# Performance work log

Hardware: AMD Instinct MI355X
Metric: run time of the kernel (lower is better)

## Reference

```python
import jax, jax.numpy as jnp
import numpy as np

NH, NKV, D = 16, 8, 128
HID = 2048
EPS = 1e-6
ROPE_BASE = 10000.0
T = 2048


def setup_inputs() -> dict:
    key = jax.random.key(0)
    k1, k2, k3 = jax.random.split(key, 3)
    return {
        "positions": jnp.arange(T, dtype=jnp.int32),
        "hidden_states": jax.random.normal(k1, (T, HID), dtype=jnp.float32),
        "w_qkv": jax.random.normal(k2, (HID, (NH + 2 * NKV) * D), dtype=jnp.float32) * 0.02,
        "w_o": jax.random.normal(k3, (NH * D, HID), dtype=jnp.float32) * 0.02,
        "q_norm_w": jnp.ones((D,), dtype=jnp.float32),
        "k_norm_w": jnp.ones((D,), dtype=jnp.float32),
    }


def _rmsnorm(x, w):
    # per-head RMSNorm over last dim (head_dim)
    return x * jax.lax.rsqrt(jnp.mean(x * x, axis=-1, keepdims=True) + EPS) * w


def reference(positions, hidden_states, w_qkv, w_o, q_norm_w, k_norm_w):
    t = hidden_states.shape[0]
    scale = D ** -0.5

    # fused QKV projection, then split
    qkv = hidden_states @ w_qkv                       # [T, (NH+2*NKV)*D]
    q, k, v = jnp.split(qkv, [NH * D, (NH + NKV) * D], axis=-1)
    q = q.reshape(t, NH, D)
    k = k.reshape(t, NKV, D)
    v = v.reshape(t, NKV, D)

    # per-head QK RMSNorm (Qwen3)
    q = _rmsnorm(q, q_norm_w)
    k = _rmsnorm(k, k_norm_w)

    # RoPE (neox style: rotate half-split pairs)
    inv_freq = 1.0 / (ROPE_BASE ** (jnp.arange(0, D, 2, dtype=jnp.float32) / D))
    freqs = positions.astype(jnp.float32)[:, None] * inv_freq  # [T, D/2]
    cos = jnp.cos(freqs)[:, None, :]                   # [T, 1, D/2]
    sin = jnp.sin(freqs)[:, None, :]

    def rope(x):
        x1, x2 = jnp.split(x, 2, axis=-1)
        return jnp.concatenate([x1 * cos - x2 * sin, x2 * cos + x1 * sin], axis=-1)

    q = rope(q)
    k = rope(k)

    # GQA: repeat kv heads
    g = NH // NKV
    kr = jnp.repeat(k, g, axis=1)                      # [T, NH, D]
    vr = jnp.repeat(v, g, axis=1)

    # causal attention
    scores = jnp.einsum('thd,shd->hts', q, kr) * scale  # [NH, T, T]
    causal = jnp.tril(jnp.ones((t, t), dtype=bool))
    scores = jnp.where(causal[None], scores, -jnp.inf)
    probs = jax.nn.softmax(scores, axis=-1)
    o = jnp.einsum('hts,shd->thd', probs, vr).reshape(t, NH * D)

    return o @ w_o
```

## Files before the change

### kernel.cpp

```cpp
#include <hip/hip_runtime.h>
#include <math.h>

#define T_TOK 2048
#define HIDDEN 2048
#define NH 16
#define NKV 8
#define DH 128

typedef unsigned short u16;
typedef __attribute__((ext_vector_type(8))) short bf16x8;
typedef __attribute__((ext_vector_type(4))) float f32x4;

__device__ __forceinline__ u16 f2bf(float f) {
  union { float f; unsigned u; } x; x.f = f;
  unsigned r = (x.u + 0x7fffu + ((x.u >> 16) & 1u)) >> 16;
  return (u16)r;
}

__device__ __forceinline__ float bf2f(u16 v) {
  union { unsigned u; float f; } x; x.u = ((unsigned)v) << 16;
  return x.f;
}

__device__ __forceinline__ void gload16(const void* g, void* l) {
  __builtin_amdgcn_global_load_lds((const __attribute__((address_space(1))) void*)g,
                                   (__attribute__((address_space(3))) void*)l,
                                   16, 0, 0);
}

__global__ __launch_bounds__(256) void prepass(const float* __restrict__ hidden,
                                               const float* __restrict__ w_qkv,
                                               const float* __restrict__ w_o,
                                               u16* __restrict__ Xb,
                                               u16* __restrict__ WqkvT,
                                               u16* __restrict__ WoT) {
  __shared__ float tile[64][65];
  const int b = blockIdx.x;
  if (b < 4096) {
    int i = b * 256 + threadIdx.x;
    float4 v = ((const float4*)hidden)[i];
    ushort4 o;
    o.x = f2bf(v.x); o.y = f2bf(v.y); o.z = f2bf(v.z); o.w = f2bf(v.w);
    ((ushort4*)Xb)[i] = o;
    return;
  }
  const float* in; u16* out; int R, Cdim, c0, r0;
  if (b < 6144) {
    int bb = b - 4096;
    in = w_qkv; out = WqkvT; R = 2048; Cdim = 4096;
    c0 = (bb & 63) * 64; r0 = (bb >> 6) * 64;
  } else {
    int bb = b - 6144;
    in = w_o; out = WoT; R = 2048; Cdim = 2048;
    c0 = (bb & 31) * 64; r0 = (bb >> 5) * 64;
  }
  const int tx = threadIdx.x & 63, ty = threadIdx.x >> 6;
#pragma unroll
  for (int i = 0; i < 64; i += 4)
    tile[ty + i][tx] = in[(size_t)(r0 + ty + i) * Cdim + c0 + tx];
  __syncthreads();
#pragma unroll
  for (int i = 0; i < 64; i += 4)
    out[(size_t)(c0 + ty + i) * R + r0 + tx] = f2bf(tile[tx][ty + i]);
}

__global__ __launch_bounds__(256) void add_parts2(const u16* __restrict__ a,
                                                  const u16* __restrict__ b,
                                                  float* __restrict__ o, int n4) {
  int i = blockIdx.x * blockDim.x + threadIdx.x;
  if (i < n4) {
    ushort4 x = ((const ushort4*)a)[i], y = ((const ushort4*)b)[i];
    float4 z;
    z.x = bf2f(x.x) + bf2f(y.x);
    z.y = bf2f(x.y) + bf2f(y.y);
    z.z = bf2f(x.z) + bf2f(y.z);
    z.w = bf2f(x.w) + bf2f(y.w);
    ((float4*)o)[i] = z;
  }
}

__global__ __launch_bounds__(256) void rope_vt(const u16* __restrict__ qkv,
                                               const int* __restrict__ pos,
                                               const float* __restrict__ qw,
                                               const float* __restrict__ kw,
                                               u16* __restrict__ Qg,
                                               u16* __restrict__ Kg,
                                               u16* __restrict__ Vt,
                                               unsigned* __restrict__ counter) {
  __shared__ float tile[64][65];
  const int b = blockIdx.x;
  if (b < 12288) {
    const int wave = threadIdx.x >> 6, j = threadIdx.x & 63;
    const int idx = b * 4 + wave;
    const int t = idx & 2047, slot = idx >> 11;
    const float QSC = 0.088388347648318447f * 1.4426950408889634f;
    const size_t base_i = (size_t)t * 4096 + slot * 128;
    float x1 = bf2f(qkv[base_i + j]);
    float x2 = bf2f(qkv[base_i + j + 64]);
    float ss = x1 * x1 + x2 * x2;
#pragma unroll
    for (int m = 1; m < 64; m <<= 1) ss += __shfl_xor(ss, m);
    float r = rsqrtf(ss * (1.0f / 128.0f) + 1e-6f);
    const bool isq = slot < NH;
    const float* w = isq ? qw : kw;
    float xn1 = x1 * r * w[j], xn2 = x2 * r * w[j + 64];
    float fp = (float)pos[t];
    float inv_freq = exp2f(-(float)j * (13.287712379549449f / 64.0f));
    float ang = fp * inv_freq;
    float sn, cs;
    sincosf(ang, &sn, &cs);
    float o1 = xn1 * cs - xn2 * sn;
    float o2 = xn2 * cs + xn1 * sn;
    if (isq) {
      size_t base = ((size_t)slot * T_TOK + t) * DH;
      Qg[base + j] = f2bf(o1 * QSC); Qg[base + 64 + j] = f2bf(o2 * QSC);
    } else {
      size_t base = ((size_t)(slot - NH) * T_TOK + t) * DH;
      Kg[base + j] = f2bf(o1); Kg[base + 64 + j] = f2bf(o2);
    }
    return;
  }
  if (b == 12288 && threadIdx.x == 0) *counter = 0u;
  const int bb = b - 12288;
  const int h = bb & 7, rest = bb >> 3;
  const int t0 = (rest & 31) * 64, d0 = (rest >> 5) * 64;
  const int tx = threadIdx.x & 63, ty = threadIdx.x >> 6;
#pragma unroll
  for (int i = 0; i < 64; i += 4) {
    size_t gi = (size_t)(t0 + ty + i) * 4096 + (NH + NKV) * DH + h * DH + d0 + tx;
    tile[ty + i][tx] = bf2f(qkv[gi]);
  }
  __syncthreads();
#pragma unroll
  for (int i = 0; i < 64; i += 4)
    Vt[((size_t)h * DH + d0 + ty + i) * T_TOK + t0 + tx] = f2bf(tile[tx][ty + i]);
}

__global__ __launch_bounds__(512, 2) void gemm128x256(const u16* __restrict__ A,
                                                      const u16* __restrict__ Bt,
                                                      void* __restrict__ Cout,
                                                      int M, int N, int K,
                                                      int lda, int ldb, int obf16) {
  __shared__ __attribute__((aligned(128))) char lds[98304];

  const int nx = N >> 8, ny = M >> 7;
  const int flat = blockIdx.x;
  const int per = gridDim.x >> 3;
  const int swz = (flat & 7) * per + (flat >> 3);
  const int by = swz % ny;
  const int rest = swz / ny;
  const int bx = rest % nx;
  const int bz = rest / nx;
  const int m0 = by << 7, n0 = bx << 8;
  A += (size_t)bz * K;
  Bt += (size_t)bz * K;

  const int tid = threadIdx.x;
  const int wave = tid >> 6, lane = tid & 63;
  const int l15 = lane & 15, quad = lane >> 4;
  const int wr = wave >> 2, wc = wave & 3;

  size_t aoff;
  {
    int chunk = tid;
    int line = chunk >> 3;
    int ls8 = (chunk & 7) ^ (line & 7);
    int row = line * 2 + (ls8 >> 2);
    int ks = ls8 & 3;
    aoff = (size_t)(m0 + row) * lda + ks * 8;
  }
  size_t boff[2];
#pragma unroll
  for (int c = 0; c < 2; ++c) {
    int chunk = c * 512 + tid;
    int line = chunk >> 3;
    int ls8 = (chunk & 7) ^ (line & 7);
    int row = line * 2 + (ls8 >> 2);
    int ks = ls8 & 3;
    boff[c] = (size_t)(n0 + row) * ldb + ks * 8;
  }

#define STAGE(tt) do {                                                   \
    char* da = lds + ((tt) & 3) * 8192 + wave * 1024;                    \
    char* db = lds + 32768 + ((tt) & 3) * 16384 + wave * 1024;           \
    const int kk = (tt) * 32;                                            \
    gload16(A + aoff + kk, da);                                          \
    gload16(Bt + boff[0] + kk, db);                                      \
    gload16(Bt + boff[1] + kk, db + 8192);                               \
  } while (0)

  const int fragoff = (l15 >> 1) * 128 +
                      (((((l15 & 1) << 2) | quad) ^ ((l15 >> 1) & 7)) << 4);

  const f32x4 zero = {0.f, 0.f, 0.f, 0.f};
  f32x4 acc[4][4];
#pragma unroll
  for (int i = 0; i < 4; ++i)
#pragma unroll
    for (int j = 0; j < 4; ++j) acc[i][j] = zero;

  const int NT = K >> 5;
  STAGE(0); STAGE(1); STAGE(2);
  asm volatile("s_waitcnt vmcnt(6)" ::: "memory");
  __builtin_amdgcn_s_barrier();

  for (int t = 0; t < NT; ++t) {
    const char* As = lds + (t & 3) * 8192 + wr * 4096 + fragoff;
    const char* Bs = lds + 32768 + (t & 3) * 16384 + wc * 4096 + fragoff;
    bf16x8 af[4], bfr[4];
#pragma unroll
    for (int mt = 0; mt < 4; ++mt) af[mt] = *(const bf16x8*)(As + mt * 1024);
#pragma unroll
    for (int nt = 0; nt < 4; ++nt) bfr[nt] = *(const bf16x8*)(Bs + nt * 1024);

    if (t + 3 < NT) STAGE(t + 3);

    __builtin_amdgcn_s_setprio(1);
#pragma unroll
    for (int mt = 0; mt < 4; ++mt)
#pragma unroll
      for (int nt = 0; nt < 4; ++nt)
        acc[mt][nt] = __builtin_amdgcn_mfma_f32_16x16x32_bf16(af[mt], bfr[nt], acc[mt][nt], 0, 0, 0);
    __builtin_amdgcn_s_setprio(0);

    const int rem = NT - 1 - t;
    if (rem >= 3)      asm volatile("s_waitcnt vmcnt(6)" ::: "memory");
    else if (rem == 2) asm volatile("s_waitcnt vmcnt(3)" ::: "memory");
    else if (rem == 1) asm volatile("s_waitcnt vmcnt(0)" ::: "memory");
    if (rem > 0) __builtin_amdgcn_s_barrier();
  }
#undef STAGE

  if (obf16) {
    u16* C = (u16*)Cout + (size_t)bz * M * N;
#pragma unroll
    for (int mt = 0; mt < 4; ++mt)
#pragma unroll
      for (int nt = 0; nt < 4; ++nt)
#pragma unroll
        for (int r = 0; r < 4; ++r)
          C[(size_t)(m0 + wr * 64 + mt * 16 + quad * 4 + r) * N + n0 + wc * 64 + nt * 16 + l15] =
              f2bf(acc[mt][nt][r]);
  } else {
    float* C = (float*)Cout + (size_t)bz * M * N;
#pragma unroll
    for (int mt = 0; mt < 4; ++mt)
#pragma unroll
      for (int nt = 0; nt < 4; ++nt)
#pragma unroll
        for (int r = 0; r < 4; ++r)
          C[(size_t)(m0 + wr * 64 + mt * 16 + quad * 4 + r) * N + n0 + wc * 64 + nt * 16 + l15] =
              acc[mt][nt][r];
  }
}

__global__ __launch_bounds__(256) void attn_kernel(const u16* __restrict__ Qg,
                                                   const u16* __restrict__ Kg,
                                                   const u16* __restrict__ Vtg,
                                                   float* __restrict__ Opart,
                                                   float* __restrict__ Lpart,
                                                   unsigned* __restrict__ counter) {
  __shared__ u16 Klds[2][64 * 128];
  __shared__ u16 Vlds[2][128 * 64];
  __shared__ u16 Plds[4][16 * 72];
  __shared__ unsigned item_s;
  const int wave = threadIdx.x >> 6, lane = threadIdx.x & 63;
  const int l15 = lane & 15, quad = lane >> 4;
  u16* Pw = &Plds[wave][0];
  const f32x4 zero = {0.f, 0.f, 0.f, 0.f};
  const float4 zero4 = {0.f, 0.f, 0.f, 0.f};

#define STAGEKV(jj, sl) do {                                            \
    u16* Kd = &Klds[sl][0]; u16* Vd = &Vlds[sl][0];                     \
    _Pragma("unroll")                                                   \
    for (int c = 0; c < 4; ++c) {                                       \
      int chunk = wave * 4 + c;                                         \
      int sL = chunk * 64 + lane;                                       \
      { int ss = sL >> 4;                                               \
        int g = (sL & 15) ^ (ss & 15);                                  \
        gload16(Kh + ((size_t)((jj) * 64 + ss)) * DH + g * 8, Kd + chunk * 512); } \
      { int d = sL >> 3;                                                \
        int g = (sL & 7) ^ (d & 7);                                     \
        gload16(Vh + (size_t)d * T_TOK + (jj) * 64 + g * 8, Vd + chunk * 512); } \
    } } while (0)

  for (;;) {
    __syncthreads();
    if (threadIdx.x == 0) item_s = atomicAdd(counter, 1u);
    __syncthreads();
    const unsigned item = item_s;
    if (item >= 1024u) break;
    const int qt = 31 - (int)(item >> 5);
    const int s  = (int)(item >> 4) & 1;
    const int h  = (int)item & 15;
    const int kvh = h >> 1;
    const int slot = (h * 32 + qt) * 2 + s;
    const int j0 = s ? (qt + 2) >> 1 : 0;
    const int j1 = s ? qt + 1 : (qt + 2) >> 1;

    float* Oslot = Opart + (size_t)slot * (64 * 128);

    if (j0 >= j1) {
      for (int t = threadIdx.x; t < 64 * 128 / 4; t += 256) ((float4*)Oslot)[t] = zero4;
      if (threadIdx.x < 64) Lpart[slot * 64 + threadIdx.x] = 0.f;
      continue;
    }

    const u16* Qh = Qg + (size_t)h * T_TOK * DH;
    const u16* Kh = Kg + (size_t)kvh * T_TOK * DH;
    const u16* Vh = Vtg + (size_t)kvh * DH * T_TOK;
    const int qrow0 = qt * 64 + wave * 16;

    bf16x8 qf[4];
#pragma unroll
    for (int ks = 0; ks < 4; ++ks)
      qf[ks] = *(const bf16x8*)(Qh + (size_t)(qrow0 + l15) * DH + ks * 32 + quad * 8);

    f32x4 oacc[8];
#pragma unroll
    for (int i = 0; i < 8; ++i) oacc[i] = zero;
    float l_i[4] = {0.f, 0.f, 0.f, 0.f};

    STAGEKV(j0, 0);
    asm volatile("s_waitcnt vmcnt(0)" ::: "memory");
    __builtin_amdgcn_s_barrier();

    for (int j = j0; j < j1; ++j) {
      const int sl = (j - j0) & 1;
      if (j + 1 < j1) STAGEKV(j + 1, sl ^ 1);
      const u16* Kl = &Klds[sl][0];
      const u16* Vl = &Vlds[sl][0];

      f32x4 sacc[4];
#pragma unroll
      for (int nt = 0; nt < 4; ++nt) sacc[nt] = zero;
      __builtin_amdgcn_s_setprio(1);
#pragma unroll
      for (int nt = 0; nt < 4; ++nt) {
        int sr = nt * 16 + l15;
#pragma unroll
        for (int ks = 0; ks < 4; ++ks) {
          bf16x8 kf = *(const bf16x8*)&Kl[sr * 128 + (((ks * 4 + quad) ^ (sr & 15)) * 8)];
          sacc[nt] = __builtin_amdgcn_mfma_f32_16x16x32_bf16(qf[ks], kf, sacc[nt], 0, 0, 0);
        }
      }
      __builtin_amdgcn_s_setprio(0);

      if (j == qt) {
#pragma unroll
        for (int nt = 0; nt < 4; ++nt)
#pragma unroll
          for (int r = 0; r < 4; ++r) {
            int col = j * 64 + nt * 16 + l15;
            int row = qrow0 + quad * 4 + r;
            if (col > row) sacc[nt][r] = -INFINITY;
          }
      }

#pragma unroll
      for (int nt = 0; nt < 4; ++nt)
#pragma unroll
        for (int r = 0; r < 4; ++r) {
          float pv = exp2f(sacc[nt][r]);
          unsigned u = __float_as_uint(pv);
          Pw[(quad * 4 + r) * 72 + nt * 16 + l15] = (u16)(u >> 16);
          l_i[r] += __uint_as_float(u & 0xffff0000u);
        }

      bf16x8 pf[2];
#pragma unroll
      for (int ks = 0; ks < 2; ++ks)
        pf[ks] = *(const bf16x8*)&Pw[l15 * 72 + ks * 32 + quad * 8];
      __builtin_amdgcn_s_setprio(1);
#pragma unroll
      for (int ot = 0; ot < 8; ++ot) {
        int d = ot * 16 + l15;
#pragma unroll
        for (int ks = 0; ks < 2; ++ks) {
          bf16x8 vf = *(const bf16x8*)&Vl[d * 64 + (((ks * 4 + quad) ^ (d & 7)) * 8)];
          oacc[ot] = __builtin_amdgcn_mfma_f32_16x16x32_bf16(pf[ks], vf, oacc[ot], 0, 0, 0);
        }
      }
      __builtin_amdgcn_s_setprio(0);

      if (j + 1 < j1) {
        asm volatile("s_waitcnt vmcnt(0)" ::: "memory");
        __builtin_amdgcn_s_barrier();
      }
    }

#pragma unroll
    for (int ot = 0; ot < 8; ++ot)
#pragma unroll
      for (int r = 0; r < 4; ++r)
        Oslot[(wave * 16 + quad * 4 + r) * 128 + ot * 16 + l15] = oacc[ot][r];
#pragma unroll
    for (int msk = 1; msk < 16; msk <<= 1)
#pragma unroll
      for (int r = 0; r < 4; ++r) l_i[r] += __shfl_xor(l_i[r], msk);
    if (l15 == 0) {
#pragma unroll
      for (int r = 0; r < 4; ++r)
        Lpart[slot * 64 + wave * 16 + quad * 4 + r] = l_i[r];
    }
  }
#undef STAGEKV
}

__global__ __launch_bounds__(256) void attn_merge(const float* __restrict__ Opart,
                                                  const float* __restrict__ Lpart,
                                                  u16* __restrict__ Og) {
  const int b = blockIdx.x;
  const int h = b & 15, qt = b >> 4;
  const int slot0 = (h * 32 + qt) * 2, slot1 = slot0 + 1;
  const float4* O0 = (const float4*)(Opart + (size_t)slot0 * (64 * 128));
  const float4* O1 = (const float4*)(Opart + (size_t)slot1 * (64 * 128));
#pragma unroll
  for (int it = 0; it < 8; ++it) {
    int idx = it * 256 + threadIdx.x;
    int r = idx >> 5, c4 = idx & 31;
    float rl = 1.0f / (Lpart[slot0 * 64 + r] + Lpart[slot1 * 64 + r]);
    float4 a = O0[idx], c = O1[idx];
    int row = qt * 64 + r, col = c4 * 4;
    u16* dst = Og + (size_t)row * (NH * DH) + h * DH + col;
    dst[0] = f2bf((a.x + c.x) * rl);
    dst[1] = f2bf((a.y + c.y) * rl);
    dst[2] = f2bf((a.z + c.z) * rl);
    dst[3] = f2bf((a.w + c.w) * rl);
  }
}

extern "C" void kernel_launch(void* const* d_in, const int* in_sizes, int n_in,
                              void* d_out, int out_size, void* d_ws, size_t ws_size,
                              hipStream_t stream) {
  (void)in_sizes; (void)n_in; (void)out_size; (void)ws_size;
  const int* positions = (const int*)d_in[0];
  const float* hidden  = (const float*)d_in[1];
  const float* w_qkv   = (const float*)d_in[2];
  const float* w_o     = (const float*)d_in[3];
  const float* q_norm  = (const float*)d_in[4];
  const float* k_norm  = (const float*)d_in[5];
  float* out = (float*)d_out;

  char* ws = (char*)d_ws;
  u16*   Xb    = (u16*)(ws);
  u16*   WqkvT = (u16*)(ws + ( 8ull << 20));
  u16*   WoT   = (u16*)(ws + (24ull << 20));
  u16*   P0    = (u16*)(ws + (32ull << 20));
  u16*   Qg    = (u16*)(ws + ( 8ull << 20));
  u16*   Kg    = (u16*)(ws + (16ull << 20));
  u16*   Vt    = (u16*)(ws + (20ull << 20));
  u16*   AttnO = (u16*)(ws + (80ull << 20));
  float* Opart = (float*)(ws + (32ull << 20));
  float* Lpart = (float*)(ws);
  unsigned* ctr = (unsigned*)(ws + (512ull << 10));
  u16*   G2P   = (u16*)(ws + (32ull << 20));

  prepass<<<dim3(7168), 256, 0, stream>>>(hidden, w_qkv, w_o, Xb, WqkvT, WoT);

  gemm128x256<<<dim3(256), 512, 0, stream>>>(
      Xb, WqkvT, P0, T_TOK, 4096, HIDDEN, HIDDEN, HIDDEN, 1);

  rope_vt<<<dim3(12288 + 512), 256, 0, stream>>>(P0, positions,
                                                 q_norm, k_norm, Qg, Kg, Vt, ctr);

  attn_kernel<<<dim3(512), 256, 0, stream>>>(Qg, Kg, Vt, Opart, Lpart, ctr);
  attn_merge<<<dim3(512), 256, 0, stream>>>(Opart, Lpart, AttnO);

  gemm128x256<<<dim3(256), 512, 0, stream>>>(
      AttnO, WoT, G2P, T_TOK, HIDDEN, 1024, NH * DH, NH * DH, 1);
  const int n4 = T_TOK * HIDDEN / 4;
  add_parts2<<<dim3(n4 / 256), 256, 0, stream>>>(
      G2P, G2P + (size_t)T_TOK * HIDDEN, out, n4);
}
```

Baseline: 241.8 us.

## Keep P in registers via transposed S MFMA, single-buffer V, raise attention occupancy

Swaps the MFMA operands for QK^T so each lane holds a key column of scores. The exponentiated probabilities can then be packed straight into bf16 register fragments for the PV MFMA, removing the per-wave P LDS round trip. V staging drops to a single buffer issued at the start of each iteration, with a partial vmcnt wait and barrier before PV. LDS shrinks enough to allow launch_bounds(256,4), and the persistent grid grows from 512 to 768 blocks. The trade-off is an extra barrier per iteration, V loads that are less overlapped, and 8-byte split V reads from LDS.

```diff
diff --git a/kernel.cpp b/kernel.cpp
--- a/kernel.cpp
+++ b/kernel.cpp
@@ -254,34 +254,40 @@
   }
 }
 
-__global__ __launch_bounds__(256) void attn_kernel(const u16* __restrict__ Qg,
-                                                   const u16* __restrict__ Kg,
-                                                   const u16* __restrict__ Vtg,
-                                                   float* __restrict__ Opart,
-                                                   float* __restrict__ Lpart,
-                                                   unsigned* __restrict__ counter) {
+__global__ __launch_bounds__(256, 4) void attn_kernel(const u16* __restrict__ Qg,
+                                                      const u16* __restrict__ Kg,
+                                                      const u16* __restrict__ Vtg,
+                                                      float* __restrict__ Opart,
+                                                      float* __restrict__ Lpart,
+                                                      unsigned* __restrict__ counter) {
   __shared__ u16 Klds[2][64 * 128];
-  __shared__ u16 Vlds[2][128 * 64];
-  __shared__ u16 Plds[4][16 * 72];
+  __shared__ u16 Vlds[128 * 64];
   __shared__ unsigned item_s;
   const int wave = threadIdx.x >> 6, lane = threadIdx.x & 63;
   const int l15 = lane & 15, quad = lane >> 4;
-  u16* Pw = &Plds[wave][0];
   const f32x4 zero = {0.f, 0.f, 0.f, 0.f};
   const float4 zero4 = {0.f, 0.f, 0.f, 0.f};
 
-#define STAGEKV(jj, sl) do {                                            \
-    u16* Kd = &Klds[sl][0]; u16* Vd = &Vlds[sl][0];                     \
+#define STAGEK(jj, sl) do {                                             \
+    u16* Kd = &Klds[sl][0];                                             \
     _Pragma("unroll")                                                   \
     for (int c = 0; c < 4; ++c) {                                       \
       int chunk = wave * 4 + c;                                         \
       int sL = chunk * 64 + lane;                                       \
-      { int ss = sL >> 4;                                               \
-        int g = (sL & 15) ^ (ss & 15);                                  \
-        gload16(Kh + ((size_t)((jj) * 64 + ss)) * DH + g * 8, Kd + chunk * 512); } \
-      { int d = sL >> 3;                                                \
-        int g = (sL & 7) ^ (d & 7);                                     \
-        gload16(Vh + (size_t)d * T_TOK + (jj) * 64 + g * 8, Vd + chunk * 512); } \
+      int ss = sL >> 4;                                                 \
+      int g = (sL & 15) ^ (ss & 15);                                    \
+      gload16(Kh + ((size_t)((jj) * 64 + ss)) * DH + g * 8, Kd + chunk * 512); \
+    } } while (0)
+
+#define STAGEV(jj) do {                                                 \
+    u16* Vd = &Vlds[0];                                                 \
+    _Pragma("unroll")                                                   \
+    for (int c = 0; c < 4; ++c) {                                       \
+      int chunk = wave * 4 + c;                                         \
+      int sL = chunk * 64 + lane;                                       \
+      int d = sL >> 3;                                                  \
+      int g = (sL & 7) ^ (d & 7);                                       \
+      gload16(Vh + (size_t)d * T_TOK + (jj) * 64 + g * 8, Vd + chunk * 512); \
     } } while (0)
 
   for (;;) {
@@ -319,17 +325,18 @@
     f32x4 oacc[8];
 #pragma unroll
     for (int i = 0; i < 8; ++i) oacc[i] = zero;
-    float l_i[4] = {0.f, 0.f, 0.f, 0.f};
-
-    STAGEKV(j0, 0);
+    float l_acc = 0.f;
+
+    STAGEK(j0, 0);
     asm volatile("s_waitcnt vmcnt(0)" ::: "memory");
     __builtin_amdgcn_s_barrier();
 
     for (int j = j0; j < j1; ++j) {
       const int sl = (j - j0) & 1;
-      if (j + 1 < j1) STAGEKV(j + 1, sl ^ 1);
+      STAGEV(j);
+      const bool more = (j + 1 < j1);
+      if (more) STAGEK(j + 1, sl ^ 1);
       const u16* Kl = &Klds[sl][0];
-      const u16* Vl = &Vlds[sl][0];
 
       f32x4 sacc[4];
 #pragma unroll
@@ -341,49 +348,56 @@
 #pragma unroll
         for (int ks = 0; ks < 4; ++ks) {
           bf16x8 kf = *(const bf16x8*)&Kl[sr * 128 + (((ks * 4 + quad) ^ (sr & 15)) * 8)];
-          sacc[nt] = __builtin_amdgcn_mfma_f32_16x16x32_bf16(qf[ks], kf, sacc[nt], 0, 0, 0);
+          sacc[nt] = __builtin_amdgcn_mfma_f32_16x16x32_bf16(kf, qf[ks], sacc[nt], 0, 0, 0);
         }
       }
       __builtin_amdgcn_s_setprio(0);
 
       if (j == qt) {
+        int q = qrow0 + l15;
 #pragma unroll
         for (int nt = 0; nt < 4; ++nt)
 #pragma unroll
           for (int r = 0; r < 4; ++r) {
-            int col = j * 64 + nt * 16 + l15;
-            int row = qrow0 + quad * 4 + r;
-            if (col > row) sacc[nt][r] = -INFINITY;
+            int k = j * 64 + nt * 16 + quad * 4 + r;
+            if (k > q) sacc[nt][r] = -INFINITY;
           }
       }
 
-#pragma unroll
-      for (int nt = 0; nt < 4; ++nt)
-#pragma unroll
-        for (int r = 0; r < 4; ++r) {
-          float pv = exp2f(sacc[nt][r]);
-          unsigned u = __float_as_uint(pv);
-          Pw[(quad * 4 + r) * 72 + nt * 16 + l15] = (u16)(u >> 16);
-          l_i[r] += __uint_as_float(u & 0xffff0000u);
+      union { unsigned d[4]; bf16x8 v; } pa[2];
+#pragma unroll
+      for (int ks = 0; ks < 2; ++ks)
+#pragma unroll
+        for (int w = 0; w < 4; ++w) {
+          int nt = ks * 2 + (w >> 1), rp = (w & 1) * 2;
+          unsigned ulo = __float_as_uint(exp2f(sacc[nt][rp]));
+          unsigned uhi = __float_as_uint(exp2f(sacc[nt][rp + 1]));
+          l_acc += __uint_as_float(ulo & 0xffff0000u) + __uint_as_float(uhi & 0xffff0000u);
+          pa[ks].d[w] = (ulo >> 16) | (uhi & 0xffff0000u);
         }
 
-      bf16x8 pf[2];
-#pragma unroll
-      for (int ks = 0; ks < 2; ++ks)
-        pf[ks] = *(const bf16x8*)&Pw[l15 * 72 + ks * 32 + quad * 8];
+      if (more) asm volatile("s_waitcnt vmcnt(4)" ::: "memory");
+      else      asm volatile("s_waitcnt vmcnt(0)" ::: "memory");
+      __builtin_amdgcn_s_barrier();
+
       __builtin_amdgcn_s_setprio(1);
 #pragma unroll
       for (int ot = 0; ot < 8; ++ot) {
         int d = ot * 16 + l15;
 #pragma unroll
         for (int ks = 0; ks < 2; ++ks) {
-          bf16x8 vf = *(const bf16x8*)&Vl[d * 64 + (((ks * 4 + quad) ^ (d & 7)) * 8)];
-          oacc[ot] = __builtin_amdgcn_mfma_f32_16x16x32_bf16(pf[ks], vf, oacc[ot], 0, 0, 0);
+          union { unsigned long long q[2]; bf16x8 v; } vf;
+          int g0 = (ks * 4 + (quad >> 1)) ^ (d & 7);
+          int g1 = (ks * 4 + 2 + (quad >> 1)) ^ (d & 7);
+          int sub = (quad & 1) * 4;
+          vf.q[0] = *(const unsigned long long*)&Vlds[d * 64 + g0 * 8 + sub];
+          vf.q[1] = *(const unsigned long long*)&Vlds[d * 64 + g1 * 8 + sub];
+          oacc[ot] = __builtin_amdgcn_mfma_f32_16x16x32_bf16(pa[ks].v, vf.v, oacc[ot], 0, 0, 0);
         }
       }
       __builtin_amdgcn_s_setprio(0);
 
-      if (j + 1 < j1) {
+      if (more) {
         asm volatile("s_waitcnt vmcnt(0)" ::: "memory");
         __builtin_amdgcn_s_barrier();
       }
@@ -394,17 +408,13 @@
 #pragma unroll
       for (int r = 0; r < 4; ++r)
         Oslot[(wave * 16 + quad * 4 + r) * 128 + ot * 16 + l15] = oacc[ot][r];
-#pragma unroll
-    for (int msk = 1; msk < 16; msk <<= 1)
-#pragma unroll
-      for (int r = 0; r < 4; ++r) l_i[r] += __shfl_xor(l_i[r], msk);
-    if (l15 == 0) {
-#pragma unroll
-      for (int r = 0; r < 4; ++r)
-        Lpart[slot * 64 + wave * 16 + quad * 4 + r] = l_i[r];
-    }
-  }
-#undef STAGEKV
+    l_acc += __shfl_xor(l_acc, 16);
+    l_acc += __shfl_xor(l_acc, 32);
+    if (quad == 0)
+      Lpart[slot * 64 + wave * 16 + l15] = l_acc;
+  }
+#undef STAGEK
+#undef STAGEV
 }
 
 __global__ __launch_bounds__(256) void attn_merge(const float* __restrict__ Opart,
@@ -464,7 +474,7 @@
   rope_vt<<<dim3(12288 + 512), 256, 0, stream>>>(P0, positions,
                                                  q_norm, k_norm, Qg, Kg, Vt, ctr);
 
-  attn_kernel<<<dim3(512), 256, 0, stream>>>(Qg, Kg, Vt, Opart, Lpart, ctr);
+  attn_kernel<<<dim3(768), 256, 0, stream>>>(Qg, Kg, Vt, Opart, Lpart, ctr);
   attn_merge<<<dim3(512), 256, 0, stream>>>(Opart, Lpart, AttnO);
 
   gemm128x256<<<dim3(256), 512, 0, stream>>>(
```

Measured after the change: 258.2 us. 1.07x slower.

## Compute transposed S tile so P stays in registers, dropping LDS round-trip

Applied to the files above, without the earlier changes.

Swaps the MFMA operands for the QK^T product so each lane holds scores for one query row across key positions. That lets the exponentiated probabilities be packed straight into the bf16 A-operand for the PV MFMA, removing the per-wave P scratch buffer in LDS, its store/load round-trip and the row-sum shuffle reduction. To match the new key ordering inside each packed fragment, the V transpose kernel permutes token columns when writing Vt. The causal mask and the row-sum reduction are rewritten for the transposed layout. Correctness depends on the V permutation exactly matching the MFMA register layout.

```diff
diff --git a/kernel.cpp b/kernel.cpp
--- a/kernel.cpp
+++ b/kernel.cpp
@@ -131,9 +131,10 @@
     tile[ty + i][tx] = bf2f(qkv[gi]);
   }
   __syncthreads();
+  const int sx = ((tx >> 5) * 2 + ((tx >> 2) & 1)) * 16 + ((tx >> 3) & 3) * 4 + (tx & 3);
 #pragma unroll
   for (int i = 0; i < 64; i += 4)
-    Vt[((size_t)h * DH + d0 + ty + i) * T_TOK + t0 + tx] = f2bf(tile[tx][ty + i]);
+    Vt[((size_t)h * DH + d0 + ty + i) * T_TOK + t0 + tx] = f2bf(tile[sx][ty + i]);
 }
 
 __global__ __launch_bounds__(512, 2) void gemm128x256(const u16* __restrict__ A,
@@ -262,11 +263,9 @@
                                                    unsigned* __restrict__ counter) {
   __shared__ u16 Klds[2][64 * 128];
   __shared__ u16 Vlds[2][128 * 64];
-  __shared__ u16 Plds[4][16 * 72];
   __shared__ unsigned item_s;
   const int wave = threadIdx.x >> 6, lane = threadIdx.x & 63;
   const int l15 = lane & 15, quad = lane >> 4;
-  u16* Pw = &Plds[wave][0];
   const f32x4 zero = {0.f, 0.f, 0.f, 0.f};
   const float4 zero4 = {0.f, 0.f, 0.f, 0.f};
 
@@ -319,7 +318,7 @@
     f32x4 oacc[8];
 #pragma unroll
     for (int i = 0; i < 8; ++i) oacc[i] = zero;
-    float l_i[4] = {0.f, 0.f, 0.f, 0.f};
+    float l_acc = 0.f;
 
     STAGEKV(j0, 0);
     asm volatile("s_waitcnt vmcnt(0)" ::: "memory");
@@ -327,7 +326,8 @@
 
     for (int j = j0; j < j1; ++j) {
       const int sl = (j - j0) & 1;
-      if (j + 1 < j1) STAGEKV(j + 1, sl ^ 1);
+      const bool more = (j + 1 < j1);
+      if (more) STAGEKV(j + 1, sl ^ 1);
       const u16* Kl = &Klds[sl][0];
       const u16* Vl = &Vlds[sl][0];
 
@@ -341,36 +341,34 @@
 #pragma unroll
         for (int ks = 0; ks < 4; ++ks) {
           bf16x8 kf = *(const bf16x8*)&Kl[sr * 128 + (((ks * 4 + quad) ^ (sr & 15)) * 8)];
-          sacc[nt] = __builtin_amdgcn_mfma_f32_16x16x32_bf16(qf[ks], kf, sacc[nt], 0, 0, 0);
+          sacc[nt] = __builtin_amdgcn_mfma_f32_16x16x32_bf16(kf, qf[ks], sacc[nt], 0, 0, 0);
         }
       }
       __builtin_amdgcn_s_setprio(0);
 
       if (j == qt) {
+        int q = qrow0 + l15;
 #pragma unroll
         for (int nt = 0; nt < 4; ++nt)
 #pragma unroll
           for (int r = 0; r < 4; ++r) {
-            int col = j * 64 + nt * 16 + l15;
-            int row = qrow0 + quad * 4 + r;
-            if (col > row) sacc[nt][r] = -INFINITY;
+            int k = j * 64 + nt * 16 + quad * 4 + r;
+            if (k > q) sacc[nt][r] = -INFINITY;
           }
       }
 
-#pragma unroll
-      for (int nt = 0; nt < 4; ++nt)
-#pragma unroll
-        for (int r = 0; r < 4; ++r) {
-          float pv = exp2f(sacc[nt][r]);
-          unsigned u = __float_as_uint(pv);
-          Pw[(quad * 4 + r) * 72 + nt * 16 + l15] = (u16)(u >> 16);
-          l_i[r] += __uint_as_float(u & 0xffff0000u);
+      union { unsigned d[4]; bf16x8 v; } pa[2];
+#pragma unroll
+      for (int ks = 0; ks < 2; ++ks)
+#pragma unroll
+        for (int w = 0; w < 4; ++w) {
+          int nt = ks * 2 + (w >> 1), rp = (w & 1) * 2;
+          unsigned ulo = __float_as_uint(exp2f(sacc[nt][rp]));
+          unsigned uhi = __float_as_uint(exp2f(sacc[nt][rp + 1]));
+          l_acc += __uint_as_float(ulo & 0xffff0000u) + __uint_as_float(uhi & 0xffff0000u);
+          pa[ks].d[w] = (ulo >> 16) | (uhi & 0xffff0000u);
         }
 
-      bf16x8 pf[2];
-#pragma unroll
-      for (int ks = 0; ks < 2; ++ks)
-        pf[ks] = *(const bf16x8*)&Pw[l15 * 72 + ks * 32 + quad * 8];
       __builtin_amdgcn_s_setprio(1);
 #pragma unroll
       for (int ot = 0; ot < 8; ++ot) {
@@ -378,12 +376,12 @@
 #pragma unroll
         for (int ks = 0; ks < 2; ++ks) {
           bf16x8 vf = *(const bf16x8*)&Vl[d * 64 + (((ks * 4 + quad) ^ (d & 7)) * 8)];
-          oacc[ot] = __builtin_amdgcn_mfma_f32_16x16x32_bf16(pf[ks], vf, oacc[ot], 0, 0, 0);
+          oacc[ot] = __builtin_amdgcn_mfma_f32_16x16x32_bf16(pa[ks].v, vf, oacc[ot], 0, 0, 0);
         }
       }
       __builtin_amdgcn_s_setprio(0);
 
-      if (j + 1 < j1) {
+      if (more) {
         asm volatile("s_waitcnt vmcnt(0)" ::: "memory");
         __builtin_amdgcn_s_barrier();
       }
@@ -394,15 +392,10 @@
 #pragma unroll
       for (int r = 0; r < 4; ++r)
         Oslot[(wave * 16 + quad * 4 + r) * 128 + ot * 16 + l15] = oacc[ot][r];
-#pragma unroll
-    for (int msk = 1; msk < 16; msk <<= 1)
-#pragma unroll
-      for (int r = 0; r < 4; ++r) l_i[r] += __shfl_xor(l_i[r], msk);
-    if (l15 == 0) {
-#pragma unroll
-      for (int r = 0; r < 4; ++r)
-        Lpart[slot * 64 + wave * 16 + quad * 4 + r] = l_i[r];
-    }
+    l_acc += __shfl_xor(l_acc, 16);
+    l_acc += __shfl_xor(l_acc, 32);
+    if (quad == 0)
+      Lpart[slot * 64 + wave * 16 + l15] = l_acc;
   }
 #undef STAGEKV
 }
```

New measurement: 240.6 us. No clear change (-0.5%).
